# Performance work log

Measured on AMD Instinct MI355X. Metric: run time of the kernel, lower is better.

The kernel has to match this reference:

```python
import jax, jax.numpy as jnp
import numpy as np

B, T, C = 128, 384, 256
H, KV, D = 4, 2, 64          # n_head, n_kv_head, head_dim
REP = H // KV                # query heads per kv head
BLOCK_SIZE = 384


def setup_inputs() -> dict:
    key = jax.random.key(0)
    k0, k1, k2, k3, k4 = jax.random.split(key, 5)
    scale = 0.02
    return {
        "x":  jax.random.normal(k0, (B, T, C), jnp.float32),
        "Wq": jax.random.normal(k1, (C, H * D), jnp.float32) * scale,
        "Wk": jax.random.normal(k2, (C, KV * D), jnp.float32) * scale,
        "Wv": jax.random.normal(k3, (C, KV * D), jnp.float32) * scale,
        "Wo": jax.random.normal(k4, (C, C), jnp.float32) * scale,
    }


def _rope_tables(t_len):
    inv_freq = 1.0 / (10000.0 ** (jnp.arange(0, D, 2, dtype=jnp.float32) / D))
    t = jnp.arange(t_len, dtype=jnp.float32)
    freqs = jnp.outer(t, inv_freq)            # [T, D/2]
    emb = jnp.concatenate([freqs, freqs], -1)  # [T, D]
    return jnp.cos(emb), jnp.sin(emb)


def _rotate_half(x):
    h = x.shape[-1] // 2
    return jnp.concatenate([-x[..., h:], x[..., :h]], -1)


def _apply_rope(x, cos, sin):
    # x: [B, heads, T, D]; cos/sin: [T, D]
    return x * cos[None, None] + _rotate_half(x) * sin[None, None]


def reference(x, Wq, Wk, Wv, Wo):
    b, t, c = x.shape
    q = (x @ Wq).reshape(b, t, H, D).transpose(0, 2, 1, 3)   # [B,H,T,D]
    k = (x @ Wk).reshape(b, t, KV, D).transpose(0, 2, 1, 3)  # [B,KV,T,D]
    v = (x @ Wv).reshape(b, t, KV, D).transpose(0, 2, 1, 3)

    cos, sin = _rope_tables(t)
    q = _apply_rope(q, cos, sin)
    k = _apply_rope(k, cos, sin)

    # GQA: group query heads by kv head instead of repeat_interleave on K/V.
    qg = q.reshape(b, KV, REP, t, D)
    scores = jnp.einsum('bgrtd,bgsd->bgrts', qg, k) / jnp.sqrt(jnp.float32(D))
    causal = jnp.tril(jnp.ones((t, t), dtype=bool))
    scores = jnp.where(causal, scores, jnp.finfo(scores.dtype).min)
    p = jax.nn.softmax(scores, axis=-1)
    y = jnp.einsum('bgrts,bgsd->bgrtd', p, v)                 # [B,KV,REP,T,D]
    y = y.reshape(b, H, t, D).transpose(0, 2, 1, 3).reshape(b, t, c)
    return y @ Wo
```

## Files before the change

kernel.cpp:

```cpp
#include <hip/hip_runtime.h>
#include <hip/hip_bf16.h>

#define BB 128
#define TT 384
#define CC 256
#define HH 4
#define KVH 2
#define QKVW 512
#define MROWS (BB * TT)

#define CVT_BLOCKS 6144

typedef __attribute__((ext_vector_type(8))) short short8;
typedef __attribute__((ext_vector_type(4))) float float4v;

__device__ __forceinline__ unsigned short f2b(float f) {
    union { float f; unsigned u; } v; v.f = f;
    unsigned u = v.u;
    unsigned r = (u + 0x7fffu + ((u >> 16) & 1u)) >> 16;
    return (unsigned short)r;
}
__device__ __forceinline__ float4v mfma16(short8 a, short8 b, float4v c) {
    return __builtin_amdgcn_mfma_f32_16x16x32_bf16(a, b, c, 0, 0, 0);
}
__device__ __forceinline__ void g2lds16(const void* g, void* l) {
    __builtin_amdgcn_global_load_lds(
        (const __attribute__((address_space(1))) unsigned int*)g,
        (__attribute__((address_space(3))) unsigned int*)l, 16, 0, 0);
}
__device__ __forceinline__ unsigned pk2bf(float a, float b) {
    union { float f; unsigned u; } x, y; x.f = a; y.f = b;
    return __builtin_amdgcn_perm(y.u + 0x8000u, x.u + 0x8000u, 0x07060302u);
}

__global__ void prep_kernel(const float* __restrict__ x, unsigned short* __restrict__ xb,
                            const float* __restrict__ Wq, const float* __restrict__ Wk,
                            const float* __restrict__ Wv, const float* __restrict__ Wo,
                            unsigned short* __restrict__ WqkvT, unsigned short* __restrict__ WoT,
                            float* __restrict__ cosT, float* __restrict__ sinT) {
    if (blockIdx.x < CVT_BLOCKS) {
        size_t e = ((size_t)blockIdx.x * 256 + threadIdx.x) * 8;
        const float4* p = (const float4*)(x + e);
        float4 v0 = p[0], v1 = p[1];
        short8 w;
        w[0]=(short)f2b(v0.x); w[1]=(short)f2b(v0.y); w[2]=(short)f2b(v0.z); w[3]=(short)f2b(v0.w);
        w[4]=(short)f2b(v1.x); w[5]=(short)f2b(v1.y); w[6]=(short)f2b(v1.z); w[7]=(short)f2b(v1.w);
        *(short8*)(xb + e) = w;
        return;
    }
    int idx = (blockIdx.x - CVT_BLOCKS) * 256 + threadIdx.x;
    const int N1 = QKVW * CC;
    const int N2 = N1 + CC * CC;
    const int N3 = N2 + TT * 32;
    if (idx < N1) {
        int n = idx >> 8, k = idx & 255;
        float w;
        if (n < 256)      w = Wq[k * 256 + n];
        else if (n < 384) w = Wk[k * 128 + (n - 256)];
        else              w = Wv[k * 128 + (n - 384)];
        WqkvT[n * 256 + k] = f2b(w);
    } else if (idx < N2) {
        int i = idx - N1; int n = i >> 8, k = i & 255;
        WoT[n * 256 + k] = f2b(Wo[k * 256 + n]);
    } else if (idx < N3) {
        int i = idx - N2;
        int t = i >> 5, f = i & 31;
        double invf = exp2(-(double)f / 32.0 * 13.287712379549449);
        double ang = (double)t * invf;
        cosT[t * 32 + f] = (float)cos(ang);
        sinT[t * 32 + f] = (float)sin(ang);
    }
}

__global__ __launch_bounds__(256) void gemm_qkv_kernel(
    const unsigned short* __restrict__ A, const unsigned short* __restrict__ BT,
    unsigned short* __restrict__ Qr, unsigned short* __restrict__ Kr,
    unsigned short* __restrict__ Vt,
    const float* __restrict__ cosT, const float* __restrict__ sinT)
{
    __shared__ __align__(16) unsigned short As[128 * 32];
    __shared__ __align__(16) unsigned short Bs[128 * 32];
    const int tid  = threadIdx.x;
    const int lane = tid & 63;
    const int quad = lane >> 4, l16 = lane & 15;
    const int wave = tid >> 6;
    const int mt = ((blockIdx.x >> 5) << 3) | (blockIdx.x & 7);
    const int nt = (blockIdx.x >> 3) & 3;
    const int mbase = mt * 128, nbase = nt * 128;
    const int wmb = (wave >> 1) * 64, wnb = (wave & 1) * 64;

    float4v acc[4][4] = {};
    const int r0 = tid >> 2, kc = (tid & 3) * 8;
    const int ldsW = (tid & ~63) * 16;
    const unsigned short* gA0 = A  + (size_t)(mbase + r0) * CC + kc;
    const unsigned short* gB0 = BT + (size_t)(nbase + r0) * CC + kc;

    for (int kt = 0; kt < CC; kt += 32) {
        __syncthreads();
        g2lds16(gA0 + kt,                  (char*)As + ldsW);
        g2lds16(gA0 + kt + (size_t)64*CC,  (char*)As + 4096 + ldsW);
        g2lds16(gB0 + kt,                  (char*)Bs + ldsW);
        g2lds16(gB0 + kt + (size_t)64*CC,  (char*)Bs + 4096 + ldsW);
        __syncthreads();

        short8 af[4], bf_[4];
        #pragma unroll
        for (int i = 0; i < 4; i++)
            af[i] = *(const short8*)&As[(wmb + i * 16 + l16) * 32 + quad * 8];
        #pragma unroll
        for (int i = 0; i < 4; i++)
            bf_[i] = *(const short8*)&Bs[(wnb + i * 16 + l16) * 32 + quad * 8];
        #pragma unroll
        for (int i = 0; i < 4; i++)
            #pragma unroll
            for (int j = 0; j < 4; j++)
                acc[i][j] = mfma16(af[i], bf_[j], acc[i][j]);
    }

    const int gn0 = nbase + wnb;
    const int gm0 = mbase + wmb;
    if (gn0 < 384) {
        const bool isq = (gn0 < 256);
        const int  hh  = isq ? (gn0 >> 6) : ((gn0 - 256) >> 6);
        const float qs = isq ? 0.18033688011112042f : 1.0f;
        #pragma unroll
        for (int i = 0; i < 4; i++) {
            #pragma unroll
            for (int r = 0; r < 4; r++) {
                int gm = gm0 + i * 16 + quad * 4 + r;
                int b = gm / TT, t = gm - b * TT;
                unsigned short* dst = isq
                    ? (Qr + (((size_t)b * HH  + hh) * TT + t) * 64)
                    : (Kr + (((size_t)b * KVH + hh) * TT + t) * 64);
                #pragma unroll
                for (int j = 0; j < 2; j++) {
                    int f = j * 16 + l16;
                    float cs = cosT[t * 32 + f], sn = sinT[t * 32 + f];
                    float a  = acc[i][j][r],     c2 = acc[i][j + 2][r];
                    dst[f]      = f2b((a * cs - c2 * sn) * qs);
                    dst[f + 32] = f2b((c2 * cs + a * sn) * qs);
                }
            }
        }
    } else {
        const int g = (gn0 - 384) >> 6;
        #pragma unroll
        for (int i = 0; i < 4; i++) {
            #pragma unroll
            for (int r = 0; r < 4; r++) {
                int gm = gm0 + i * 16 + quad * 4 + r;
                int b = gm / TT, s = gm - b * TT;
                int s6 = s & 63;
                int sig = (s6 & 15) * 4 + (s6 >> 4);
                unsigned short* dst = Vt + (((size_t)b * KVH + g) * 6 + (s >> 6)) * 4096 + sig;
                #pragma unroll
                for (int j = 0; j < 4; j++)
                    dst[(j * 16 + l16) * 64] = f2b(acc[i][j][r]);
            }
        }
    }
}

__global__ __launch_bounds__(256) void gemm_out_kernel(
    const unsigned short* __restrict__ A, const unsigned short* __restrict__ BT,
    float* __restrict__ C)
{
    __shared__ __align__(16) unsigned short As[128 * 32];
    __shared__ __align__(16) unsigned short Bs[128 * 32];
    const int tid  = threadIdx.x;
    const int lane = tid & 63;
    const int quad = lane >> 4, l16 = lane & 15;
    const int wave = tid >> 6;
    const int mt = ((blockIdx.x >> 4) << 3) | (blockIdx.x & 7);
    const int nt = (blockIdx.x >> 3) & 1;
    const int mbase = mt * 128, nbase = nt * 128;
    const int wmb = (wave >> 1) * 64, wnb = (wave & 1) * 64;

    float4v acc[4][4] = {};
    const int r0 = tid >> 2, kc = (tid & 3) * 8;
    const int ldsW = (tid & ~63) * 16;
    const unsigned short* gA0 = A  + (size_t)(mbase + r0) * CC + kc;
    const unsigned short* gB0 = BT + (size_t)(nbase + r0) * CC + kc;

    for (int kt = 0; kt < CC; kt += 32) {
        __syncthreads();
        g2lds16(gA0 + kt,                  (char*)As + ldsW);
        g2lds16(gA0 + kt + (size_t)64*CC,  (char*)As + 4096 + ldsW);
        g2lds16(gB0 + kt,                  (char*)Bs + ldsW);
        g2lds16(gB0 + kt + (size_t)64*CC,  (char*)Bs + 4096 + ldsW);
        __syncthreads();

        short8 af[4], bf_[4];
        #pragma unroll
        for (int i = 0; i < 4; i++)
            af[i] = *(const short8*)&As[(wmb + i * 16 + l16) * 32 + quad * 8];
        #pragma unroll
        for (int i = 0; i < 4; i++)
            bf_[i] = *(const short8*)&Bs[(wnb + i * 16 + l16) * 32 + quad * 8];
        #pragma unroll
        for (int i = 0; i < 4; i++)
            #pragma unroll
            for (int j = 0; j < 4; j++)
                acc[i][j] = mfma16(af[i], bf_[j], acc[i][j]);
    }
    #pragma unroll
    for (int i = 0; i < 4; i++)
        #pragma unroll
        for (int j = 0; j < 4; j++)
            #pragma unroll
            for (int r = 0; r < 4; r++)
                C[(size_t)(mbase + wmb + i * 16 + quad * 4 + r) * CC + nbase + wnb + j * 16 + l16]
                    = acc[i][j][r];
}

__global__ __launch_bounds__(256, 3) void attn_kernel(
    const unsigned short* __restrict__ Qr, const unsigned short* __restrict__ Kr,
    const unsigned short* __restrict__ Vt, unsigned short* __restrict__ y)
{
    __shared__ __align__(16) unsigned short Ks[2][64 * 64];
    __shared__ __align__(16) unsigned short Vs[2][64 * 64];
    __shared__ __align__(16) unsigned short Ps[4][32 * 64];

    const int tid  = threadIdx.x;
    const int lane = tid & 63;
    const int wave = tid >> 6;
    const int quad = lane >> 4, l16 = lane & 15;

    const int xc  = blockIdx.x & 7;
    const int jj  = blockIdx.x >> 3;
    const int p   = jj % 3;
    const int bg  = (jj / 3) * 8 + xc;
    const int g   = bg & 1, b = bg >> 1;
    const int h   = g * 2 + (wave >> 1);
    const int qtA = 5 - p, qtB = p;
    const int qbA = qtA * 64 + (wave & 1) * 32;
    const int qbB = qtB * 64 + (wave & 1) * 32;

    short8 qf[2][2][2];
    #pragma unroll
    for (int t = 0; t < 2; t++) {
        int qb = t ? qbB : qbA;
        #pragma unroll
        for (int mi = 0; mi < 2; mi++)
            #pragma unroll
            for (int half = 0; half < 2; half++)
                qf[t][mi][half] = *(const short8*)(Qr
                    + (((size_t)b * HH + h) * TT + qb + mi * 16 + l16) * 64
                    + half * 32 + quad * 8);
    }

    float4v acc[2][2][4] = {};
    float4v accl[2][2]   = {};
    short8 ones;
    #pragma unroll
    for (int j = 0; j < 8; j++) ones[j] = (short)0x3F80;

    const unsigned short* Kbase = Kr + ((size_t)b * KVH + g) * TT * 64;
    const unsigned short* Vbase = Vt + ((size_t)b * KVH + g) * 6 * 4096;
    char* Pw = (char*)&Ps[wave][0];
    const int ldsWave = (tid & ~63) * 16;
    int gc0, gc1;
    { int L0 = tid;       gc0 = ((L0 & ~7) | ((L0 & 7) ^ ((L0 >> 3) & 7))) * 8;
      int L1 = 256 + tid; gc1 = ((L1 & ~7) | ((L1 & 7) ^ ((L1 >> 3) & 7))) * 8; }

    auto stage = [&](int bi, int kt) {
        const unsigned short* kB = Kbase + (size_t)kt * 4096;
        const unsigned short* vB = Vbase + (size_t)kt * 4096;
        g2lds16(kB + gc0, (char*)&Ks[bi][0] + ldsWave);
        g2lds16(kB + gc1, (char*)&Ks[bi][0] + 4096 + ldsWave);
        g2lds16(vB + gc0, (char*)&Vs[bi][0] + ldsWave);
        g2lds16(vB + gc1, (char*)&Vs[bi][0] + 4096 + ldsWave);
    };

    auto computeTile = [&](int t, const unsigned short* Kc, const unsigned short* Vc,
                           bool domask) {
        float4v s_[2][4];
        #pragma unroll
        for (int js = 0; js < 4; js++) {
            int srow = js * 16 + l16, sw = srow & 7;
            short8 kb0 = *(const short8*)((const char*)Kc + srow * 128 + ((quad ^ sw) * 16));
            short8 kb1 = *(const short8*)((const char*)Kc + srow * 128 + (((4 + quad) ^ sw) * 16));
            #pragma unroll
            for (int mi = 0; mi < 2; mi++) {
                float4v z = {};
                z = mfma16(qf[t][mi][0], kb0, z);
                s_[mi][js] = mfma16(qf[t][mi][1], kb1, z);
            }
        }
        if (domask) {
            #pragma unroll
            for (int mi = 0; mi < 2; mi++)
                #pragma unroll
                for (int js = 0; js < 4; js++) {
                    int coll = js * 16 + l16;
                    #pragma unroll
                    for (int r = 0; r < 4; r++) {
                        int rowl = (wave & 1) * 32 + mi * 16 + quad * 4 + r;
                        if (coll > rowl) s_[mi][js][r] = -1e30f;
                    }
                }
        }
        #pragma unroll
        for (int mi = 0; mi < 2; mi++)
            #pragma unroll
            for (int r = 0; r < 4; r++) {
                float e0 = __builtin_amdgcn_exp2f(s_[mi][0][r]);
                float e1 = __builtin_amdgcn_exp2f(s_[mi][1][r]);
                float e2 = __builtin_amdgcn_exp2f(s_[mi][2][r]);
                float e3 = __builtin_amdgcn_exp2f(s_[mi][3][r]);
                unsigned long long d =
                    (unsigned long long)pk2bf(e0, e1) |
                    ((unsigned long long)pk2bf(e2, e3) << 32);
                int rho = mi * 16 + quad * 4 + r;
                int ch  = l16 ^ (((quad * 4 + r) & 7) << 1);
                *(unsigned long long*)(Pw + rho * 128 + ch * 8) = d;
            }
        short8 pa[2][2];
        #pragma unroll
        for (int mi = 0; mi < 2; mi++)
            #pragma unroll
            for (int half = 0; half < 2; half++) {
                int chp = (2 * (half * 4 + quad)) ^ ((l16 & 7) << 1);
                pa[mi][half] = *(const short8*)(Pw + (mi * 16 + l16) * 128 + chp * 8);
            }
        #pragma unroll
        for (int dj = 0; dj < 4; dj++) {
            int vrow = dj * 16 + l16, sw = vrow & 7;
            short8 vb0 = *(const short8*)((const char*)Vc + vrow * 128 + ((quad ^ sw) * 16));
            short8 vb1 = *(const short8*)((const char*)Vc + vrow * 128 + (((4 + quad) ^ sw) * 16));
            #pragma unroll
            for (int mi = 0; mi < 2; mi++) {
                acc[t][mi][dj] = mfma16(pa[mi][0], vb0, acc[t][mi][dj]);
                acc[t][mi][dj] = mfma16(pa[mi][1], vb1, acc[t][mi][dj]);
            }
        }
        #pragma unroll
        for (int mi = 0; mi < 2; mi++) {
            accl[t][mi] = mfma16(pa[mi][0], ones, accl[t][mi]);
            accl[t][mi] = mfma16(pa[mi][1], ones, accl[t][mi]);
        }
    };

    stage(0, 0);
    for (int kt = 0; kt <= qtA; kt++) {
        __syncthreads();
        if (kt < qtA) stage((kt + 1) & 1, kt + 1);
        const unsigned short* Kc = &Ks[kt & 1][0];
        const unsigned short* Vc = &Vs[kt & 1][0];
        computeTile(0, Kc, Vc, kt == qtA);
        if (kt <= qtB) computeTile(1, Kc, Vc, kt == qtB);
    }

    #pragma unroll
    for (int t = 0; t < 2; t++) {
        int qb = t ? qbB : qbA;
        #pragma unroll
        for (int mi = 0; mi < 2; mi++) {
            float rinv[4];
            #pragma unroll
            for (int r = 0; r < 4; r++) rinv[r] = 1.0f / accl[t][mi][r];
            #pragma unroll
            for (int dj = 0; dj < 4; dj++)
                #pragma unroll
                for (int r = 0; r < 4; r++) {
                    int tt = qb + mi * 16 + quad * 4 + r;
                    y[((size_t)b * TT + tt) * CC + h * 64 + dj * 16 + l16]
                        = f2b(acc[t][mi][dj][r] * rinv[r]);
                }
        }
    }
}

extern "C" void kernel_launch(void* const* d_in, const int* in_sizes, int n_in,
                              void* d_out, int out_size, void* d_ws, size_t ws_size,
                              hipStream_t stream) {
    const float* x  = (const float*)d_in[0];
    const float* Wq = (const float*)d_in[1];
    const float* Wk = (const float*)d_in[2];
    const float* Wv = (const float*)d_in[3];
    const float* Wo = (const float*)d_in[4];
    float* out = (float*)d_out;

    char* ws = (char*)d_ws;
    size_t off = 0;
    unsigned short* xb = (unsigned short*)(ws + off); off += (size_t)MROWS * CC * 2;
    unsigned short* Qr = (unsigned short*)(ws + off); off += (size_t)BB * HH  * TT * 64 * 2;
    unsigned short* Kr = (unsigned short*)(ws + off); off += (size_t)BB * KVH * TT * 64 * 2;
    unsigned short* Vt = (unsigned short*)(ws + off); off += (size_t)BB * KVH * TT * 64 * 2;
    unsigned short* y  = (unsigned short*)(ws + off); off += (size_t)MROWS * CC * 2;
    unsigned short* WqkvT = (unsigned short*)(ws + off); off += (size_t)QKVW * CC * 2;
    unsigned short* WoT   = (unsigned short*)(ws + off); off += (size_t)CC * CC * 2;
    float* cosT = (float*)(ws + off); off += (size_t)TT * 32 * 4;
    float* sinT = (float*)(ws + off); off += (size_t)TT * 32 * 4;

    prep_kernel<<<CVT_BLOCKS + 816, 256, 0, stream>>>(x, xb, Wq, Wk, Wv, Wo,
                                                      WqkvT, WoT, cosT, sinT);
    gemm_qkv_kernel<<<(MROWS / 128) * 4, 256, 0, stream>>>(xb, WqkvT, Qr, Kr, Vt, cosT, sinT);
    attn_kernel<<<BB * KVH * 3, 256, 0, stream>>>(Qr, Kr, Vt, y);
    gemm_out_kernel<<<(MROWS / 128) * 2, 256, 0, stream>>>(y, WoT, out);
}
```

Before: 194.5 us.

## Process the paired query tiles sequentially to halve accumulator registers

The attention kernel no longer computes its two causal-balanced query tiles together over one shared KV sweep. It now handles them one after the other, each with its own KV loop, and prefetches KV tile 0 for the second pass at the end of the first. This halves the live Q fragments and accumulators, lowering register pressure and possibly allowing higher occupancy. The cost is that the K/V tiles covering the short tile's range are staged into LDS twice, adding one extra load and barrier per shared tile.

```diff
diff --git a/kernel.cpp b/kernel.cpp
--- a/kernel.cpp
+++ b/kernel.cpp
@@ -232,31 +232,11 @@
     const int bg  = (jj / 3) * 8 + xc;
     const int g   = bg & 1, b = bg >> 1;
     const int h   = g * 2 + (wave >> 1);
-    const int qtA = 5 - p, qtB = p;
-    const int qbA = qtA * 64 + (wave & 1) * 32;
-    const int qbB = qtB * 64 + (wave & 1) * 32;
-
-    short8 qf[2][2][2];
-    #pragma unroll
-    for (int t = 0; t < 2; t++) {
-        int qb = t ? qbB : qbA;
-        #pragma unroll
-        for (int mi = 0; mi < 2; mi++)
-            #pragma unroll
-            for (int half = 0; half < 2; half++)
-                qf[t][mi][half] = *(const short8*)(Qr
-                    + (((size_t)b * HH + h) * TT + qb + mi * 16 + l16) * 64
-                    + half * 32 + quad * 8);
-    }
-
-    float4v acc[2][2][4] = {};
-    float4v accl[2][2]   = {};
-    short8 ones;
-    #pragma unroll
-    for (int j = 0; j < 8; j++) ones[j] = (short)0x3F80;
 
     const unsigned short* Kbase = Kr + ((size_t)b * KVH + g) * TT * 64;
     const unsigned short* Vbase = Vt + ((size_t)b * KVH + g) * 6 * 4096;
+    const unsigned short* Qbase = Qr + ((size_t)b * HH + h) * TT * 64;
+    unsigned short* ybase = y + (size_t)b * TT * CC + h * 64;
     char* Pw = (char*)&Ps[wave][0];
     const int ldsWave = (tid & ~63) * 16;
     int gc0, gc1;
@@ -272,100 +252,117 @@
         g2lds16(vB + gc1, (char*)&Vs[bi][0] + 4096 + ldsWave);
     };
 
-    auto computeTile = [&](int t, const unsigned short* Kc, const unsigned short* Vc,
-                           bool domask) {
-        float4v s_[2][4];
-        #pragma unroll
-        for (int js = 0; js < 4; js++) {
-            int srow = js * 16 + l16, sw = srow & 7;
-            short8 kb0 = *(const short8*)((const char*)Kc + srow * 128 + ((quad ^ sw) * 16));
-            short8 kb1 = *(const short8*)((const char*)Kc + srow * 128 + (((4 + quad) ^ sw) * 16));
+    short8 ones;
+    #pragma unroll
+    for (int j = 0; j < 8; j++) ones[j] = (short)0x3F80;
+
+    int seq = 0;
+    stage(0, 0);
+
+    for (int tph = 0; tph < 2; tph++) {
+        const int qt = tph ? (5 - p) : p;
+        const int qb = qt * 64 + (wave & 1) * 32;
+
+        short8 qf[2][2];
+        #pragma unroll
+        for (int mi = 0; mi < 2; mi++)
+            #pragma unroll
+            for (int half = 0; half < 2; half++)
+                qf[mi][half] = *(const short8*)(Qbase
+                    + (size_t)(qb + mi * 16 + l16) * 64 + half * 32 + quad * 8);
+
+        float4v acc[2][4] = {};
+        float4v accl[2]   = {};
+
+        for (int kt = 0; kt <= qt; kt++) {
+            __syncthreads();
+            if (kt < qt)        stage((seq + 1) & 1, kt + 1);
+            else if (tph == 0)  stage((seq + 1) & 1, 0);
+            const unsigned short* Kc = &Ks[seq & 1][0];
+            const unsigned short* Vc = &Vs[seq & 1][0];
+
+            float4v s_[2][4];
+            #pragma unroll
+            for (int js = 0; js < 4; js++) {
+                int srow = js * 16 + l16, sw = srow & 7;
+                short8 kb0 = *(const short8*)((const char*)Kc + srow * 128 + ((quad ^ sw) * 16));
+                short8 kb1 = *(const short8*)((const char*)Kc + srow * 128 + (((4 + quad) ^ sw) * 16));
+                #pragma unroll
+                for (int mi = 0; mi < 2; mi++) {
+                    float4v z = {};
+                    z = mfma16(qf[mi][0], kb0, z);
+                    s_[mi][js] = mfma16(qf[mi][1], kb1, z);
+                }
+            }
+
+            if (kt == qt) {
+                #pragma unroll
+                for (int mi = 0; mi < 2; mi++)
+                    #pragma unroll
+                    for (int js = 0; js < 4; js++) {
+                        int coll = js * 16 + l16;
+                        #pragma unroll
+                        for (int r = 0; r < 4; r++) {
+                            int rowl = (wave & 1) * 32 + mi * 16 + quad * 4 + r;
+                            if (coll > rowl) s_[mi][js][r] = -1e30f;
+                        }
+                    }
+            }
+
+            #pragma unroll
+            for (int mi = 0; mi < 2; mi++)
+                #pragma unroll
+                for (int r = 0; r < 4; r++) {
+                    float e0 = __builtin_amdgcn_exp2f(s_[mi][0][r]);
+                    float e1 = __builtin_amdgcn_exp2f(s_[mi][1][r]);
+                    float e2 = __builtin_amdgcn_exp2f(s_[mi][2][r]);
+                    float e3 = __builtin_amdgcn_exp2f(s_[mi][3][r]);
+                    unsigned long long d =
+                        (unsigned long long)pk2bf(e0, e1) |
+                        ((unsigned long long)pk2bf(e2, e3) << 32);
+                    int rho = mi * 16 + quad * 4 + r;
+                    int ch  = l16 ^ (((quad * 4 + r) & 7) << 1);
+                    *(unsigned long long*)(Pw + rho * 128 + ch * 8) = d;
+                }
+
+            short8 pa[2][2];
+            #pragma unroll
+            for (int mi = 0; mi < 2; mi++)
+                #pragma unroll
+                for (int half = 0; half < 2; half++) {
+                    int chp = (2 * (half * 4 + quad)) ^ ((l16 & 7) << 1);
+                    pa[mi][half] = *(const short8*)(Pw + (mi * 16 + l16) * 128 + chp * 8);
+                }
+            #pragma unroll
+            for (int dj = 0; dj < 4; dj++) {
+                int vrow = dj * 16 + l16, sw = vrow & 7;
+                short8 vb0 = *(const short8*)((const char*)Vc + vrow * 128 + ((quad ^ sw) * 16));
+                short8 vb1 = *(const short8*)((const char*)Vc + vrow * 128 + (((4 + quad) ^ sw) * 16));
+                #pragma unroll
+                for (int mi = 0; mi < 2; mi++) {
+                    acc[mi][dj] = mfma16(pa[mi][0], vb0, acc[mi][dj]);
+                    acc[mi][dj] = mfma16(pa[mi][1], vb1, acc[mi][dj]);
+                }
+            }
             #pragma unroll
             for (int mi = 0; mi < 2; mi++) {
-                float4v z = {};
-                z = mfma16(qf[t][mi][0], kb0, z);
-                s_[mi][js] = mfma16(qf[t][mi][1], kb1, z);
-            }
+                accl[mi] = mfma16(pa[mi][0], ones, accl[mi]);
+                accl[mi] = mfma16(pa[mi][1], ones, accl[mi]);
+            }
+            seq++;
         }
-        if (domask) {
-            #pragma unroll
-            for (int mi = 0; mi < 2; mi++)
-                #pragma unroll
-                for (int js = 0; js < 4; js++) {
-                    int coll = js * 16 + l16;
-                    #pragma unroll
-                    for (int r = 0; r < 4; r++) {
-                        int rowl = (wave & 1) * 32 + mi * 16 + quad * 4 + r;
-                        if (coll > rowl) s_[mi][js][r] = -1e30f;
-                    }
-                }
-        }
-        #pragma unroll
-        for (int mi = 0; mi < 2; mi++)
-            #pragma unroll
-            for (int r = 0; r < 4; r++) {
-                float e0 = __builtin_amdgcn_exp2f(s_[mi][0][r]);
-                float e1 = __builtin_amdgcn_exp2f(s_[mi][1][r]);
-                float e2 = __builtin_amdgcn_exp2f(s_[mi][2][r]);
-                float e3 = __builtin_amdgcn_exp2f(s_[mi][3][r]);
-                unsigned long long d =
-                    (unsigned long long)pk2bf(e0, e1) |
-                    ((unsigned long long)pk2bf(e2, e3) << 32);
-                int rho = mi * 16 + quad * 4 + r;
-                int ch  = l16 ^ (((quad * 4 + r) & 7) << 1);
-                *(unsigned long long*)(Pw + rho * 128 + ch * 8) = d;
-            }
-        short8 pa[2][2];
-        #pragma unroll
-        for (int mi = 0; mi < 2; mi++)
-            #pragma unroll
-            for (int half = 0; half < 2; half++) {
-                int chp = (2 * (half * 4 + quad)) ^ ((l16 & 7) << 1);
-                pa[mi][half] = *(const short8*)(Pw + (mi * 16 + l16) * 128 + chp * 8);
-            }
-        #pragma unroll
-        for (int dj = 0; dj < 4; dj++) {
-            int vrow = dj * 16 + l16, sw = vrow & 7;
-            short8 vb0 = *(const short8*)((const char*)Vc + vrow * 128 + ((quad ^ sw) * 16));
-            short8 vb1 = *(const short8*)((const char*)Vc + vrow * 128 + (((4 + quad) ^ sw) * 16));
-            #pragma unroll
-            for (int mi = 0; mi < 2; mi++) {
-                acc[t][mi][dj] = mfma16(pa[mi][0], vb0, acc[t][mi][dj]);
-                acc[t][mi][dj] = mfma16(pa[mi][1], vb1, acc[t][mi][dj]);
-            }
-        }
-        #pragma unroll
-        for (int mi = 0; mi < 2; mi++) {
-            accl[t][mi] = mfma16(pa[mi][0], ones, accl[t][mi]);
-            accl[t][mi] = mfma16(pa[mi][1], ones, accl[t][mi]);
-        }
-    };
-
-    stage(0, 0);
-    for (int kt = 0; kt <= qtA; kt++) {
-        __syncthreads();
-        if (kt < qtA) stage((kt + 1) & 1, kt + 1);
-        const unsigned short* Kc = &Ks[kt & 1][0];
-        const unsigned short* Vc = &Vs[kt & 1][0];
-        computeTile(0, Kc, Vc, kt == qtA);
-        if (kt <= qtB) computeTile(1, Kc, Vc, kt == qtB);
-    }
-
-    #pragma unroll
-    for (int t = 0; t < 2; t++) {
-        int qb = t ? qbB : qbA;
+
         #pragma unroll
         for (int mi = 0; mi < 2; mi++) {
             float rinv[4];
             #pragma unroll
-            for (int r = 0; r < 4; r++) rinv[r] = 1.0f / accl[t][mi][r];
+            for (int r = 0; r < 4; r++) rinv[r] = 1.0f / accl[mi][r];
             #pragma unroll
             for (int dj = 0; dj < 4; dj++)
                 #pragma unroll
                 for (int r = 0; r < 4; r++) {
                     int tt = qb + mi * 16 + quad * 4 + r;
-                    y[((size_t)b * TT + tt) * CC + h * 64 + dj * 16 + l16]
-                        = f2b(acc[t][mi][dj][r] * rinv[r]);
+                    ybase[(size_t)tt * CC + dj * 16 + l16] = f2b(acc[mi][dj][r] * rinv[r]);
                 }
         }
     }
```

Result: faster. 160.7 us (-17.4%).
